# Kernel tuning notes

Hardware: AMD Instinct MI355X
Metric: run time of the kernel (lower is better)

The kernel has to match this reference:

```python
import jax, jax.numpy as jnp
import numpy as np

N, E, G = 50000, 500000, 64
DIN, ED, H1, H2, HD, OUT = 128, 32, 256, 128, 64, 8


def setup_inputs() -> dict:
    key = jax.random.key(0)
    ks = jax.random.split(key, 20)
    g = lambda i, shape: (jax.random.normal(ks[i], shape, jnp.float32) * 0.05)
    return dict(
        node_attr=jax.random.normal(ks[0], (N, DIN), jnp.float32),
        edge_attr=jax.random.normal(ks[1], (E, ED), jnp.float32),
        edge_src=jax.random.randint(ks[2], (E,), 0, N, jnp.int32),
        edge_dst=jax.random.randint(ks[3], (E,), 0, N, jnp.int32),
        batch=jnp.sort(jax.random.randint(ks[4], (N,), 0, G, jnp.int32)),
        Wl1=g(5, (DIN, H1)), bl1=jnp.zeros((H1,), jnp.float32),
        Wr1=g(6, (DIN, H1)), br1=jnp.zeros((H1,), jnp.float32),
        We1=g(7, (ED, H1)), att1=g(8, (H1,)), b1=jnp.zeros((H1,), jnp.float32),
        Wl2=g(9, (H1, H2)), bl2=jnp.zeros((H2,), jnp.float32),
        Wr2=g(10, (H1, H2)), br2=jnp.zeros((H2,), jnp.float32),
        We2=g(11, (ED, H2)), att2=g(12, (H2,)), b2=jnp.zeros((H2,), jnp.float32),
        Wd1=g(13, (H2, HD)), bd1=jnp.zeros((HD,), jnp.float32),
        bn_gamma=jnp.ones((HD,), jnp.float32), bn_beta=jnp.zeros((HD,), jnp.float32),
        bn_mean=jnp.zeros((HD,), jnp.float32), bn_var=jnp.ones((HD,), jnp.float32),
        Wd2=g(14, (HD, OUT)), bd2=jnp.zeros((OUT,), jnp.float32),
    )


def gatv2(x, src, dst, eattr, Wl, bl, Wr, br, We, att, bias, n):
    # PyG GATv2Conv, heads=1: add self-loops (fill_value='mean' for edge_attr)
    ones = jnp.ones((eattr.shape[0],), x.dtype)
    deg = jax.ops.segment_sum(ones, dst, n)
    loop_attr = jax.ops.segment_sum(eattr, dst, n) / jnp.maximum(deg, 1.0)[:, None]
    loop = jnp.arange(n, dtype=src.dtype)
    src_ = jnp.concatenate([src, loop])
    dst_ = jnp.concatenate([dst, loop])
    eattr_ = jnp.concatenate([eattr, loop_attr], axis=0)
    xl = x @ Wl + bl  # [n, C] source transform (lin_l)
    xr = x @ Wr + br  # [n, C] dest transform (lin_r)
    # edge-wise GATv2 score: a^T LeakyReLU(xl_j + xr_i + We e_ij)
    e = jax.nn.leaky_relu(xl[src_] + xr[dst_] + eattr_ @ We, 0.2) @ att  # [E+n]
    m = jax.ops.segment_max(e, dst_, n)
    w = jnp.exp(e - m[dst_])
    denom = jax.ops.segment_sum(w, dst_, n)
    alpha = w / denom[dst_]
    return jax.ops.segment_sum(alpha[:, None] * xl[src_], dst_, n) + bias


def reference(node_attr, edge_attr, edge_src, edge_dst, batch,
              Wl1, bl1, Wr1, br1, We1, att1, b1,
              Wl2, bl2, Wr2, br2, We2, att2, b2,
              Wd1, bd1, bn_gamma, bn_beta, bn_mean, bn_var, Wd2, bd2):
    x = jax.nn.relu(gatv2(node_attr, edge_src, edge_dst, edge_attr,
                          Wl1, bl1, Wr1, br1, We1, att1, b1, N))
    x = jax.nn.relu(gatv2(x, edge_src, edge_dst, edge_attr,
                          Wl2, bl2, Wr2, br2, We2, att2, b2, N))
    # global mean pool over graphs
    cnt = jax.ops.segment_sum(jnp.ones((N,), x.dtype), batch, G)
    x = jax.ops.segment_sum(x, batch, G) / jnp.maximum(cnt, 1.0)[:, None]
    x = x @ Wd1 + bd1
    # BatchNorm1d in eval mode (running stats); dropout is identity in eval
    x = (x - bn_mean) / jnp.sqrt(bn_var + 1e-5) * bn_gamma + bn_beta
    x = jax.nn.leaky_relu(x, 0.1)
    return x @ Wd2 + bd2
```

## Files before the change

### kernel.cpp

```cpp
#include <hip/hip_runtime.h>
#include <cstdint>
#include <cstddef>
#include <cmath>

constexpr int Nn = 50000;
constexpr int Ne = 500000;
constexpr int Gg = 64;
constexpr int DIN = 128, ED = 32, H1 = 256, H2 = 128, HD = 64, NOUT = 8;

typedef __attribute__((ext_vector_type(8))) short bf16x8;
typedef __attribute__((ext_vector_type(4))) float f32x4;

__device__ __forceinline__ unsigned short f2bf(float x) {
    unsigned u = __float_as_uint(x);
    u += 0x7FFFu + ((u >> 16) & 1u);
    return (unsigned short)(u >> 16);
}
__device__ __forceinline__ float bf2f(unsigned short h) {
    return __uint_as_float(((unsigned)h) << 16);
}

__global__ void count_deg_kernel(const int* __restrict__ dst, int* __restrict__ deg) {
    int e = blockIdx.x * 256 + threadIdx.x;
    if (e < Ne) atomicAdd(&deg[dst[e]], 1);
}

__global__ __launch_bounds__(1024) void scan_kernel(const int* __restrict__ deg,
                                                    int* __restrict__ row_start) {
    __shared__ int part[1024];
    int t = threadIdx.x;
    const int chunk = (Nn + 1023) / 1024;
    int lo = t * chunk;
    int hi = min(lo + chunk, Nn);
    int s = 0;
    for (int i = lo; i < hi; i++) s += deg[i];
    part[t] = s;
    __syncthreads();
    for (int off = 1; off < 1024; off <<= 1) {
        int add = (t >= off) ? part[t - off] : 0;
        __syncthreads();
        part[t] += add;
        __syncthreads();
    }
    int base = (t == 0) ? 0 : part[t - 1];
    for (int i = lo; i < hi; i++) { row_start[i] = base; base += deg[i]; }
    if (t == 0) row_start[Nn] = Ne;
}

__global__ void scatter_kernel(const int* __restrict__ dst, const int* __restrict__ row_start,
                               int* __restrict__ cursor, int* __restrict__ perm) {
    int e = blockIdx.x * 256 + threadIdx.x;
    if (e < Ne) {
        int d = dst[e];
        int p = atomicAdd(&cursor[d], 1);
        perm[row_start[d] + p] = e;
    }
}

__global__ void build_sd_kernel(const int* __restrict__ perm, const int* __restrict__ src,
                                const int* __restrict__ dst,
                                int* __restrict__ srcv, int* __restrict__ dstv) {
    int j = blockIdx.x * 256 + threadIdx.x;
    if (j < Ne) {
        int e = perm[j];
        srcv[j] = src[e];
        dstv[j] = dst[e];
    }
}

__global__ void loop_attr_kernel(const int* __restrict__ row_start, const int* __restrict__ perm,
                                 const float* __restrict__ eattr, float* __restrict__ loop_attr) {
    int tid = blockIdx.x * 256 + threadIdx.x;
    if (tid >= Nn * 8) return;
    int i = tid >> 3, q = (tid & 7) << 2;
    int r0 = row_start[i], r1 = row_start[i + 1];
    float4 s = make_float4(0.f, 0.f, 0.f, 0.f);
    for (int j = r0; j < r1; j++) {
        int e = perm[j];
        float4 v = *(const float4*)(eattr + (size_t)e * ED + q);
        s.x += v.x; s.y += v.y; s.z += v.z; s.w += v.w;
    }
    float inv = 1.0f / fmaxf((float)(r1 - r0), 1.0f);
    *(float4*)(loop_attr + (size_t)i * ED + q) =
        make_float4(s.x * inv, s.y * inv, s.z * inv, s.w * inv);
}

__global__ void cvt_split_kernel(const float* __restrict__ src,
                                 unsigned short* __restrict__ hi,
                                 unsigned short* __restrict__ lo, int n4) {
    int idx = blockIdx.x * 256 + threadIdx.x;
    if (idx >= n4) return;
    float4 v = *(const float4*)(src + (size_t)idx * 4);
    float x[4] = {v.x, v.y, v.z, v.w};
    unsigned short h[4], l[4];
#pragma unroll
    for (int c = 0; c < 4; c++) {
        h[c] = f2bf(x[c]);
        l[c] = f2bf(x[c] - bf2f(h[c]));
    }
    *(ushort4*)(hi + (size_t)idx * 4) = make_ushort4(h[0], h[1], h[2], h[3]);
    *(ushort4*)(lo + (size_t)idx * 4) = make_ushort4(l[0], l[1], l[2], l[3]);
}

__global__ void cvt_wt_kernel(const float* __restrict__ W,
                              unsigned short* __restrict__ hi,
                              unsigned short* __restrict__ lo, int K, int N) {
    int t = blockIdx.x * 256 + threadIdx.x;
    if (t >= K * N) return;
    int col = t / K, k = t % K;
    float x = W[(size_t)k * N + col];
    unsigned short h = f2bf(x);
    hi[t] = h;
    lo[t] = f2bf(x - bf2f(h));
}

template <int K, int N>
__global__ __launch_bounds__(256) void gemm_mfma_kernel(
    int M, const float* __restrict__ A,
    const unsigned short* __restrict__ wt0hi, const unsigned short* __restrict__ wt0lo,
    const float* __restrict__ bias0, float* __restrict__ C0,
    const unsigned short* __restrict__ wt1hi, const unsigned short* __restrict__ wt1lo,
    const float* __restrict__ bias1, float* __restrict__ C1) {
    const unsigned short* wthi = blockIdx.z ? wt1hi : wt0hi;
    const unsigned short* wtlo = blockIdx.z ? wt1lo : wt0lo;
    const float* bias = blockIdx.z ? bias1 : bias0;
    float* Cc = blockIdx.z ? C1 : C0;
    constexpr int KC = (K > 128) ? 128 : K;
    constexpr int P = KC + 8;
    constexpr int NT = N / 64;
    constexpr int CH = KC / 4;
    __shared__ unsigned short Ah[64 * P], Al[64 * P];
    const int tid = threadIdx.x;
    const int m0 = blockIdx.y * 64;

    const int wv = tid >> 6, lane = tid & 63;
    const int g = lane >> 4, li = lane & 15;
    const int nb = wv * (N / 4);

    f32x4 acc[4][NT];
#pragma unroll
    for (int n = 0; n < NT; n++) {
        float bc = bias[nb + n * 16 + li];
#pragma unroll
        for (int m = 0; m < 4; m++) {
            acc[m][n][0] = bc; acc[m][n][1] = bc; acc[m][n][2] = bc; acc[m][n][3] = bc;
        }
    }

    for (int kc = 0; kc < K; kc += KC) {
        for (int t = tid; t < 64 * CH; t += 256) {
            int row = t / CH, c = t % CH;
            int gr = min(m0 + row, M - 1);
            float4 v = *(const float4*)(A + (size_t)gr * K + kc + c * 4);
            unsigned short h0 = f2bf(v.x), h1 = f2bf(v.y), h2 = f2bf(v.z), h3 = f2bf(v.w);
            unsigned short l0 = f2bf(v.x - bf2f(h0)), l1 = f2bf(v.y - bf2f(h1));
            unsigned short l2 = f2bf(v.z - bf2f(h2)), l3 = f2bf(v.w - bf2f(h3));
            *(ushort4*)&Ah[row * P + c * 4] = make_ushort4(h0, h1, h2, h3);
            *(ushort4*)&Al[row * P + c * 4] = make_ushort4(l0, l1, l2, l3);
        }
        __syncthreads();

#pragma unroll
        for (int kt = 0; kt < KC / 32; kt++) {
            bf16x8 afh[4], afl[4], bfh[NT], bfl[NT];
#pragma unroll
            for (int m = 0; m < 4; m++) {
                afh[m] = *(const bf16x8*)&Ah[(m * 16 + li) * P + kt * 32 + g * 8];
                afl[m] = *(const bf16x8*)&Al[(m * 16 + li) * P + kt * 32 + g * 8];
            }
#pragma unroll
            for (int n = 0; n < NT; n++) {
                int col = nb + n * 16 + li;
                bfh[n] = *(const bf16x8*)(wthi + (size_t)col * K + kc + kt * 32 + g * 8);
                bfl[n] = *(const bf16x8*)(wtlo + (size_t)col * K + kc + kt * 32 + g * 8);
            }
#pragma unroll
            for (int m = 0; m < 4; m++)
#pragma unroll
                for (int n = 0; n < NT; n++) {
                    acc[m][n] = __builtin_amdgcn_mfma_f32_16x16x32_bf16(afh[m], bfh[n], acc[m][n], 0, 0, 0);
                    acc[m][n] = __builtin_amdgcn_mfma_f32_16x16x32_bf16(afh[m], bfl[n], acc[m][n], 0, 0, 0);
                    acc[m][n] = __builtin_amdgcn_mfma_f32_16x16x32_bf16(afl[m], bfh[n], acc[m][n], 0, 0, 0);
                }
        }
        __syncthreads();
    }

#pragma unroll
    for (int m = 0; m < 4; m++)
#pragma unroll
        for (int n = 0; n < NT; n++) {
            int col = nb + n * 16 + li;
#pragma unroll
            for (int r = 0; r < 4; r++) {
                int node = m0 + m * 16 + g * 4 + r;
                if (node < M) Cc[(size_t)node * N + col] = acc[m][n][r];
            }
        }
}

template <int C>
__global__ __launch_bounds__((C / 64) * 64) void score_mfma3_kernel(
    int count, const int* __restrict__ perm,
    const int* __restrict__ srcv, const int* __restrict__ dstv,
    const unsigned short* __restrict__ ehi, const unsigned short* __restrict__ elo,
    const float* __restrict__ xl, const float* __restrict__ xr,
    const unsigned short* __restrict__ wthi, const unsigned short* __restrict__ wtlo,
    const float* __restrict__ att, float* __restrict__ sc_out) {
    constexpr int WPB = C / 64;
    constexpr int NTHR = WPB * 64;
    __shared__ unsigned short Ah[64 * 40], Al[64 * 40];
    __shared__ float pw[WPB][64];
    const int tid = threadIdx.x;
    const int j0 = blockIdx.x * 64;

    for (int t = tid; t < 64 * 4; t += NTHR) {
        int row = t >> 2, part = t & 3;
        int j = min(j0 + row, count - 1);
        int e = perm ? perm[j] : j;
        *(uint4*)&Ah[row * 40 + part * 8] = *(const uint4*)(ehi + (size_t)e * ED + part * 8);
        *(uint4*)&Al[row * 40 + part * 8] = *(const uint4*)(elo + (size_t)e * ED + part * 8);
    }
    __syncthreads();

    const int wv = tid >> 6, lane = tid & 63;
    const int g = lane >> 4, li = lane & 15;
    const int cb = wv * 64 + g * 4;

    bf16x8 af_h[4], af_l[4];
#pragma unroll
    for (int m = 0; m < 4; m++) {
        int col = wv * 64 + m * 16 + li;
        af_h[m] = *(const bf16x8*)(wthi + (size_t)col * ED + g * 8);
        af_l[m] = *(const bf16x8*)(wtlo + (size_t)col * ED + g * 8);
    }
    float4 attv[4];
#pragma unroll
    for (int m = 0; m < 4; m++) attv[m] = *(const float4*)(att + cb + m * 16);

    int s0, d0, s1, d1, s2, d2, s3, d3;
    {
        int j;
        j = min(j0 + 0 * 16 + li, count - 1); s0 = srcv ? srcv[j] : j; d0 = dstv ? dstv[j] : j;
        j = min(j0 + 1 * 16 + li, count - 1); s1 = srcv ? srcv[j] : j; d1 = dstv ? dstv[j] : j;
        j = min(j0 + 2 * 16 + li, count - 1); s2 = srcv ? srcv[j] : j; d2 = dstv ? dstv[j] : j;
        j = min(j0 + 3 * 16 + li, count - 1); s3 = srcv ? srcv[j] : j; d3 = dstv ? dstv[j] : j;
    }

    auto pf = [&](int n, int sE, int dE, bf16x8& bh, bf16x8& bl,
                  float4 (&xlv)[4], float4 (&xrv)[4]) {
        bh = *(const bf16x8*)&Ah[(n * 16 + li) * 40 + g * 8];
        bl = *(const bf16x8*)&Al[(n * 16 + li) * 40 + g * 8];
        const float* pl = xl + (size_t)sE * C + cb;
        const float* pr = xr + (size_t)dE * C + cb;
#pragma unroll
        for (int m = 0; m < 4; m++) {
            xlv[m] = *(const float4*)(pl + m * 16);
            xrv[m] = *(const float4*)(pr + m * 16);
        }
    };
    auto comp = [&](int n, bf16x8 bh, bf16x8 bl,
                    const float4 (&xlv)[4], const float4 (&xrv)[4]) {
        f32x4 acc[4];
#pragma unroll
        for (int m = 0; m < 4; m++) {
            acc[m][0] = xlv[m].x + xrv[m].x; acc[m][1] = xlv[m].y + xrv[m].y;
            acc[m][2] = xlv[m].z + xrv[m].z; acc[m][3] = xlv[m].w + xrv[m].w;
        }
#pragma unroll
        for (int m = 0; m < 4; m++) {
            acc[m] = __builtin_amdgcn_mfma_f32_16x16x32_bf16(af_h[m], bh, acc[m], 0, 0, 0);
            acc[m] = __builtin_amdgcn_mfma_f32_16x16x32_bf16(af_h[m], bl, acc[m], 0, 0, 0);
            acc[m] = __builtin_amdgcn_mfma_f32_16x16x32_bf16(af_l[m], bh, acc[m], 0, 0, 0);
        }
        float s = 0.f;
#pragma unroll
        for (int m = 0; m < 4; m++) {
            const float av[4] = {attv[m].x, attv[m].y, attv[m].z, attv[m].w};
#pragma unroll
            for (int r = 0; r < 4; r++) {
                float z = acc[m][r];
                z = z > 0.f ? z : 0.2f * z;
                s = fmaf(z, av[r], s);
            }
        }
        s += __shfl_xor(s, 16);
        s += __shfl_xor(s, 32);
        if (lane < 16) pw[wv][n * 16 + li] = s;
    };

    bf16x8 bhA, blA, bhB, blB;
    float4 xlA[4], xrA[4], xlB[4], xrB[4];
    pf(0, s0, d0, bhA, blA, xlA, xrA);
    pf(1, s1, d1, bhB, blB, xlB, xrB);
    comp(0, bhA, blA, xlA, xrA);
    pf(2, s2, d2, bhA, blA, xlA, xrA);
    comp(1, bhB, blB, xlB, xrB);
    pf(3, s3, d3, bhB, blB, xlB, xrB);
    comp(2, bhA, blA, xlA, xrA);
    comp(3, bhB, blB, xlB, xrB);

    __syncthreads();
    if (tid < 64) {
        float s = pw[0][tid];
#pragma unroll
        for (int w = 1; w < WPB; w++) s += pw[w][tid];
        int j = j0 + tid;
        if (j < count) sc_out[j] = s;
    }
}

template <int C>
__global__ __launch_bounds__(256) void aggregate2_kernel(
    const int* __restrict__ row_start, const int* __restrict__ srcv,
    const float* __restrict__ scores, const float* __restrict__ sscore,
    const float* __restrict__ xl, const float* __restrict__ bias,
    float* __restrict__ xout) {
    constexpr int VP = C / 64;
    const int wave = threadIdx.x >> 6, lane = threadIdx.x & 63;
    const int i = blockIdx.x * 4 + wave;
    if (i >= Nn) return;
    const int r0 = row_start[i], r1 = row_start[i + 1];

    float mx = sscore[i];
    for (int j = r0 + lane; j < r1; j += 64) mx = fmaxf(mx, scores[j]);
#pragma unroll
    for (int off = 32; off >= 1; off >>= 1) mx = fmaxf(mx, __shfl_xor(mx, off));

    float l = 0.f;
    float acc[VP];
#pragma unroll
    for (int j = 0; j < VP; j++) acc[j] = 0.f;

    float wA[4], xA[4][VP];
    auto load_batch = [&](int j0, float* w, float (*x)[VP]) {
#pragma unroll
        for (int q = 0; q < 4; q++) {
            int j = min(j0 + q, r1 - 1);
            w[q] = scores[j];
            const float* p = xl + (size_t)srcv[j] * C + lane * VP;
            if constexpr (VP == 4) {
                float4 v = *(const float4*)p;
                x[q][0] = v.x; x[q][1] = v.y; x[q][2] = v.z; x[q][3] = v.w;
            } else {
                float2 v = *(const float2*)p;
                x[q][0] = v.x; x[q][1] = v.y;
            }
        }
    };
    if (r0 < r1) load_batch(r0, wA, xA);

    for (int j0 = r0; j0 < r1; j0 += 4) {
        float wB[4], xB[4][VP];
        if (j0 + 4 < r1) load_batch(j0 + 4, wB, xB);
        const int nb = min(4, r1 - j0);
        for (int q = 0; q < nb; q++) {
            float w = __expf(wA[q] - mx);
            l += w;
#pragma unroll
            for (int j = 0; j < VP; j++) acc[j] = fmaf(w, xA[q][j], acc[j]);
        }
        if (j0 + 4 < r1) {
#pragma unroll
            for (int q = 0; q < 4; q++) {
                wA[q] = wB[q];
#pragma unroll
                for (int j = 0; j < VP; j++) xA[q][j] = xB[q][j];
            }
        }
    }

    {
        float w = __expf(sscore[i] - mx);
        l += w;
        const float* p = xl + (size_t)i * C + lane * VP;
        if constexpr (VP == 4) {
            float4 v = *(const float4*)p;
            acc[0] = fmaf(w, v.x, acc[0]); acc[1] = fmaf(w, v.y, acc[1]);
            acc[2] = fmaf(w, v.z, acc[2]); acc[3] = fmaf(w, v.w, acc[3]);
        } else {
            float2 v = *(const float2*)p;
            acc[0] = fmaf(w, v.x, acc[0]); acc[1] = fmaf(w, v.y, acc[1]);
        }
    }

    float invl = 1.0f / l;
    float* xo = xout + (size_t)i * C + lane * VP;
    if constexpr (VP == 4) {
        float4 bv = *(const float4*)(bias + lane * 4);
        float4 o;
        o.x = fmaxf(fmaf(acc[0], invl, bv.x), 0.f);
        o.y = fmaxf(fmaf(acc[1], invl, bv.y), 0.f);
        o.z = fmaxf(fmaf(acc[2], invl, bv.z), 0.f);
        o.w = fmaxf(fmaf(acc[3], invl, bv.w), 0.f);
        *(float4*)xo = o;
    } else {
        float2 bv = *(const float2*)(bias + lane * 2);
        float2 o;
        o.x = fmaxf(fmaf(acc[0], invl, bv.x), 0.f);
        o.y = fmaxf(fmaf(acc[1], invl, bv.y), 0.f);
        *(float2*)xo = o;
    }
}

__global__ __launch_bounds__(128) void pool2_kernel(const float* __restrict__ x2,
                                                    const int* __restrict__ batch,
                                                    float* __restrict__ pooled,
                                                    float* __restrict__ cnt) {
    const int c = threadIdx.x;
    const int chunk = (Nn + gridDim.x - 1) / gridDim.x;
    int lo = blockIdx.x * chunk;
    int hi = min(lo + chunk, Nn);
    if (lo >= hi) return;
    int gcur = batch[lo];
    float acc = 0.f, ncnt = 0.f;
    for (int i = lo; i < hi; i++) {
        int g = batch[i];
        if (g != gcur) {
            atomicAdd(&pooled[gcur * H2 + c], acc);
            if (c == 0) atomicAdd(&cnt[gcur], ncnt);
            acc = 0.f; ncnt = 0.f; gcur = g;
        }
        acc += x2[(size_t)i * H2 + c];
        ncnt += 1.f;
    }
    atomicAdd(&pooled[gcur * H2 + c], acc);
    if (c == 0) atomicAdd(&cnt[gcur], ncnt);
}

__global__ __launch_bounds__(64) void head_kernel(
    const float* __restrict__ pooled, const float* __restrict__ cnt,
    const float* __restrict__ Wd1, const float* __restrict__ bd1,
    const float* __restrict__ gamma, const float* __restrict__ beta,
    const float* __restrict__ mean, const float* __restrict__ var,
    const float* __restrict__ Wd2, const float* __restrict__ bd2,
    float* __restrict__ out) {
    __shared__ float xm[H2];
    __shared__ float h[HD];
    int g = blockIdx.x, t = threadIdx.x;
    float c = fmaxf(cnt[g], 1.0f);
    for (int i = t; i < H2; i += 64) xm[i] = pooled[g * H2 + i] / c;
    __syncthreads();
    float a = bd1[t];
    for (int k = 0; k < H2; k++) a = fmaf(xm[k], Wd1[k * HD + t], a);
    a = (a - mean[t]) / sqrtf(var[t] + 1e-5f) * gamma[t] + beta[t];
    a = a > 0.f ? a : 0.1f * a;
    h[t] = a;
    __syncthreads();
    if (t < NOUT) {
        float o = bd2[t];
        for (int k = 0; k < HD; k++) o = fmaf(h[k], Wd2[k * NOUT + t], o);
        out[g * NOUT + t] = o;
    }
}

extern "C" void kernel_launch(void* const* d_in, const int* in_sizes, int n_in,
                              void* d_out, int out_size, void* d_ws, size_t ws_size,
                              hipStream_t stream) {
    const float* node_attr = (const float*)d_in[0];
    const float* edge_attr = (const float*)d_in[1];
    const int* edge_src = (const int*)d_in[2];
    const int* edge_dst = (const int*)d_in[3];
    const int* batch = (const int*)d_in[4];
    const float* Wl1 = (const float*)d_in[5];  const float* bl1 = (const float*)d_in[6];
    const float* Wr1 = (const float*)d_in[7];  const float* br1 = (const float*)d_in[8];
    const float* We1 = (const float*)d_in[9];  const float* att1 = (const float*)d_in[10];
    const float* b1 = (const float*)d_in[11];
    const float* Wl2 = (const float*)d_in[12]; const float* bl2 = (const float*)d_in[13];
    const float* Wr2 = (const float*)d_in[14]; const float* br2 = (const float*)d_in[15];
    const float* We2 = (const float*)d_in[16]; const float* att2 = (const float*)d_in[17];
    const float* b2 = (const float*)d_in[18];
    const float* Wd1 = (const float*)d_in[19]; const float* bd1 = (const float*)d_in[20];
    const float* bn_gamma = (const float*)d_in[21]; const float* bn_beta = (const float*)d_in[22];
    const float* bn_mean = (const float*)d_in[23];  const float* bn_var = (const float*)d_in[24];
    const float* Wd2 = (const float*)d_in[25]; const float* bd2 = (const float*)d_in[26];
    float* out = (float*)d_out;

    char* ws = (char*)d_ws;
    size_t off = 0;
    auto alloc = [&](size_t bytes) -> char* {
        char* p = ws + off;
        off = (off + bytes + 255) & ~(size_t)255;
        return p;
    };
    int* deg         = (int*)alloc((size_t)Nn * 4);
    int* row_start   = (int*)alloc((size_t)(Nn + 1) * 4);
    int* cursor      = (int*)alloc((size_t)Nn * 4);
    int* perm        = (int*)alloc((size_t)Ne * 4);
    int* srcv        = (int*)alloc((size_t)Ne * 4);
    int* dstv        = (int*)alloc((size_t)Ne * 4);
    float* loop_attr = (float*)alloc((size_t)Nn * ED * 4);
    float* scores    = (float*)alloc((size_t)Ne * 4);
    float* sscore    = (float*)alloc((size_t)Nn * 4);
    float* pooled    = (float*)alloc((size_t)Gg * H2 * 4);
    float* cnt       = (float*)alloc((size_t)Gg * 4);
    float* xlb       = (float*)alloc((size_t)Nn * H1 * 4);
    float* xrb       = (float*)alloc((size_t)Nn * H1 * 4);
    float* x1        = (float*)alloc((size_t)Nn * H1 * 4);
    unsigned short* ehi = (unsigned short*)alloc((size_t)Ne * ED * 2);
    unsigned short* elo = (unsigned short*)alloc((size_t)Ne * ED * 2);
    unsigned short* lhi = (unsigned short*)alloc((size_t)Nn * ED * 2);
    unsigned short* llo = (unsigned short*)alloc((size_t)Nn * ED * 2);
    unsigned short* w1hi = (unsigned short*)alloc((size_t)H1 * ED * 2);
    unsigned short* w1lo = (unsigned short*)alloc((size_t)H1 * ED * 2);
    unsigned short* w2hi = (unsigned short*)alloc((size_t)H2 * ED * 2);
    unsigned short* w2lo = (unsigned short*)alloc((size_t)H2 * ED * 2);
    unsigned short* wl1hi = (unsigned short*)alloc((size_t)H1 * DIN * 2);
    unsigned short* wl1lo = (unsigned short*)alloc((size_t)H1 * DIN * 2);
    unsigned short* wr1hi = (unsigned short*)alloc((size_t)H1 * DIN * 2);
    unsigned short* wr1lo = (unsigned short*)alloc((size_t)H1 * DIN * 2);
    unsigned short* wl2hi = (unsigned short*)alloc((size_t)H2 * H1 * 2);
    unsigned short* wl2lo = (unsigned short*)alloc((size_t)H2 * H1 * 2);
    unsigned short* wr2hi = (unsigned short*)alloc((size_t)H2 * H1 * 2);
    unsigned short* wr2lo = (unsigned short*)alloc((size_t)H2 * H1 * 2);

    hipMemsetAsync(deg, 0, (size_t)Nn * 4, stream);
    hipMemsetAsync(cursor, 0, (size_t)Nn * 4, stream);
    hipMemsetAsync(pooled, 0, (size_t)Gg * H2 * 4, stream);
    hipMemsetAsync(cnt, 0, (size_t)Gg * 4, stream);

    count_deg_kernel<<<(Ne + 255) / 256, 256, 0, stream>>>(edge_dst, deg);
    scan_kernel<<<1, 1024, 0, stream>>>(deg, row_start);
    scatter_kernel<<<(Ne + 255) / 256, 256, 0, stream>>>(edge_dst, row_start, cursor, perm);
    build_sd_kernel<<<(Ne + 255) / 256, 256, 0, stream>>>(perm, edge_src, edge_dst, srcv, dstv);
    loop_attr_kernel<<<(Nn * 8 + 255) / 256, 256, 0, stream>>>(row_start, perm, edge_attr, loop_attr);

    cvt_split_kernel<<<(Ne * 8 + 255) / 256, 256, 0, stream>>>(edge_attr, ehi, elo, Ne * 8);
    cvt_split_kernel<<<(Nn * 8 + 255) / 256, 256, 0, stream>>>(loop_attr, lhi, llo, Nn * 8);
    cvt_wt_kernel<<<(H1 * ED + 255) / 256, 256, 0, stream>>>(We1, w1hi, w1lo, ED, H1);
    cvt_wt_kernel<<<(H2 * ED + 255) / 256, 256, 0, stream>>>(We2, w2hi, w2lo, ED, H2);
    cvt_wt_kernel<<<(DIN * H1 + 255) / 256, 256, 0, stream>>>(Wl1, wl1hi, wl1lo, DIN, H1);
    cvt_wt_kernel<<<(DIN * H1 + 255) / 256, 256, 0, stream>>>(Wr1, wr1hi, wr1lo, DIN, H1);
    cvt_wt_kernel<<<(H1 * H2 + 255) / 256, 256, 0, stream>>>(Wl2, wl2hi, wl2lo, H1, H2);
    cvt_wt_kernel<<<(H1 * H2 + 255) / 256, 256, 0, stream>>>(Wr2, wr2hi, wr2lo, H1, H2);

    const int eb64 = (Ne + 63) / 64, nb64 = (Nn + 63) / 64;
    const int gb = (Nn + 63) / 64;

    gemm_mfma_kernel<DIN, H1><<<dim3(1, gb, 2), 256, 0, stream>>>(
        Nn, node_attr, wl1hi, wl1lo, bl1, xlb, wr1hi, wr1lo, br1, xrb);
    score_mfma3_kernel<H1><<<eb64, 256, 0, stream>>>(
        Ne, perm, srcv, dstv, ehi, elo, xlb, xrb, w1hi, w1lo, att1, scores);
    score_mfma3_kernel<H1><<<nb64, 256, 0, stream>>>(
        Nn, nullptr, nullptr, nullptr, lhi, llo, xlb, xrb, w1hi, w1lo, att1, sscore);
    aggregate2_kernel<H1><<<(Nn + 3) / 4, 256, 0, stream>>>(
        row_start, srcv, scores, sscore, xlb, b1, x1);

    gemm_mfma_kernel<H1, H2><<<dim3(1, gb, 2), 256, 0, stream>>>(
        Nn, x1, wl2hi, wl2lo, bl2, xlb, wr2hi, wr2lo, br2, xrb);
    score_mfma3_kernel<H2><<<eb64, 128, 0, stream>>>(
        Ne, perm, srcv, dstv, ehi, elo, xlb, xrb, w2hi, w2lo, att2, scores);
    score_mfma3_kernel<H2><<<nb64, 128, 0, stream>>>(
        Nn, nullptr, nullptr, nullptr, lhi, llo, xlb, xrb, w2hi, w2lo, att2, sscore);
    float* x2 = x1;
    aggregate2_kernel<H2><<<(Nn + 3) / 4, 256, 0, stream>>>(
        row_start, srcv, scores, sscore, xlb, b2, x2);

    pool2_kernel<<<256, 128, 0, stream>>>(x2, batch, pooled, cnt);
    head_kernel<<<Gg, 64, 0, stream>>>(pooled, cnt, Wd1, bd1, bn_gamma, bn_beta,
                                       bn_mean, bn_var, Wd2, bd2, out);
}
```

Measured before the change: 844.9 us.

## Fuse bf16 hi/lo split into score kernel and merge launches

Removes the separate passes that split edge and loop attributes into bf16 hi/lo arrays. The score kernel now reads fp32 attributes and does the split while staging them into shared memory. The edge and self-loop score launches are merged into one grid, and the six weight-conversion kernels become a single 2D launch. This drops the extra attribute read/write traffic and several launches. In exchange each layer's score kernel reads fp32 attributes (twice the bytes of the bf16 pair) and repeats the conversion arithmetic.

```diff
diff --git a/kernel.cpp b/kernel.cpp
--- a/kernel.cpp
+++ b/kernel.cpp
@@ -85,26 +85,22 @@
         make_float4(s.x * inv, s.y * inv, s.z * inv, s.w * inv);
 }
 
-__global__ void cvt_split_kernel(const float* __restrict__ src,
-                                 unsigned short* __restrict__ hi,
-                                 unsigned short* __restrict__ lo, int n4) {
-    int idx = blockIdx.x * 256 + threadIdx.x;
-    if (idx >= n4) return;
-    float4 v = *(const float4*)(src + (size_t)idx * 4);
-    float x[4] = {v.x, v.y, v.z, v.w};
-    unsigned short h[4], l[4];
-#pragma unroll
-    for (int c = 0; c < 4; c++) {
-        h[c] = f2bf(x[c]);
-        l[c] = f2bf(x[c] - bf2f(h[c]));
-    }
-    *(ushort4*)(hi + (size_t)idx * 4) = make_ushort4(h[0], h[1], h[2], h[3]);
-    *(ushort4*)(lo + (size_t)idx * 4) = make_ushort4(l[0], l[1], l[2], l[3]);
-}
-
-__global__ void cvt_wt_kernel(const float* __restrict__ W,
-                              unsigned short* __restrict__ hi,
-                              unsigned short* __restrict__ lo, int K, int N) {
+__global__ void cvt_wt6_kernel(
+    const float* __restrict__ We1, unsigned short* __restrict__ w1hi, unsigned short* __restrict__ w1lo,
+    const float* __restrict__ We2, unsigned short* __restrict__ w2hi, unsigned short* __restrict__ w2lo,
+    const float* __restrict__ Wl1, unsigned short* __restrict__ wl1hi, unsigned short* __restrict__ wl1lo,
+    const float* __restrict__ Wr1, unsigned short* __restrict__ wr1hi, unsigned short* __restrict__ wr1lo,
+    const float* __restrict__ Wl2, unsigned short* __restrict__ wl2hi, unsigned short* __restrict__ wl2lo,
+    const float* __restrict__ Wr2, unsigned short* __restrict__ wr2hi, unsigned short* __restrict__ wr2lo) {
+    const float* W; unsigned short *hi, *lo; int K, N;
+    switch (blockIdx.y) {
+        case 0: W = We1; hi = w1hi;  lo = w1lo;  K = ED;  N = H1; break;
+        case 1: W = We2; hi = w2hi;  lo = w2lo;  K = ED;  N = H2; break;
+        case 2: W = Wl1; hi = wl1hi; lo = wl1lo; K = DIN; N = H1; break;
+        case 3: W = Wr1; hi = wr1hi; lo = wr1lo; K = DIN; N = H1; break;
+        case 4: W = Wl2; hi = wl2hi; lo = wl2lo; K = H1;  N = H2; break;
+        default: W = Wr2; hi = wr2hi; lo = wr2lo; K = H1;  N = H2; break;
+    }
     int t = blockIdx.x * 256 + threadIdx.x;
     if (t >= K * N) return;
     int col = t / K, k = t % K;
@@ -200,26 +196,36 @@
 }
 
 template <int C>
-__global__ __launch_bounds__((C / 64) * 64) void score_mfma3_kernel(
-    int count, const int* __restrict__ perm,
+__global__ __launch_bounds__((C / 64) * 64) void score_mfma4_kernel(
+    int ecount, int eblocks, const int* __restrict__ perm,
     const int* __restrict__ srcv, const int* __restrict__ dstv,
-    const unsigned short* __restrict__ ehi, const unsigned short* __restrict__ elo,
+    const float* __restrict__ eattr, float* __restrict__ esc,
+    int ncount, const float* __restrict__ lattr, float* __restrict__ nsc,
     const float* __restrict__ xl, const float* __restrict__ xr,
     const unsigned short* __restrict__ wthi, const unsigned short* __restrict__ wtlo,
-    const float* __restrict__ att, float* __restrict__ sc_out) {
+    const float* __restrict__ att) {
     constexpr int WPB = C / 64;
     constexpr int NTHR = WPB * 64;
     __shared__ unsigned short Ah[64 * 40], Al[64 * 40];
     __shared__ float pw[WPB][64];
     const int tid = threadIdx.x;
-    const int j0 = blockIdx.x * 64;
-
-    for (int t = tid; t < 64 * 4; t += NTHR) {
-        int row = t >> 2, part = t & 3;
+    const bool selfp = (int)blockIdx.x >= eblocks;
+    const int bid = selfp ? ((int)blockIdx.x - eblocks) : (int)blockIdx.x;
+    const int count = selfp ? ncount : ecount;
+    const float* attr = selfp ? lattr : eattr;
+    float* sc_out = selfp ? nsc : esc;
+    const int j0 = bid * 64;
+
+    for (int t = tid; t < 64 * 8; t += NTHR) {
+        int row = t >> 3, c = t & 7;
         int j = min(j0 + row, count - 1);
-        int e = perm ? perm[j] : j;
-        *(uint4*)&Ah[row * 40 + part * 8] = *(const uint4*)(ehi + (size_t)e * ED + part * 8);
-        *(uint4*)&Al[row * 40 + part * 8] = *(const uint4*)(elo + (size_t)e * ED + part * 8);
+        int e = selfp ? j : perm[j];
+        float4 v = *(const float4*)(attr + (size_t)e * ED + c * 4);
+        unsigned short h0 = f2bf(v.x), h1 = f2bf(v.y), h2 = f2bf(v.z), h3 = f2bf(v.w);
+        unsigned short l0 = f2bf(v.x - bf2f(h0)), l1 = f2bf(v.y - bf2f(h1));
+        unsigned short l2 = f2bf(v.z - bf2f(h2)), l3 = f2bf(v.w - bf2f(h3));
+        *(ushort4*)&Ah[row * 40 + c * 4] = make_ushort4(h0, h1, h2, h3);
+        *(ushort4*)&Al[row * 40 + c * 4] = make_ushort4(l0, l1, l2, l3);
     }
     __syncthreads();
 
@@ -241,10 +247,14 @@
     int s0, d0, s1, d1, s2, d2, s3, d3;
     {
         int j;
-        j = min(j0 + 0 * 16 + li, count - 1); s0 = srcv ? srcv[j] : j; d0 = dstv ? dstv[j] : j;
-        j = min(j0 + 1 * 16 + li, count - 1); s1 = srcv ? srcv[j] : j; d1 = dstv ? dstv[j] : j;
-        j = min(j0 + 2 * 16 + li, count - 1); s2 = srcv ? srcv[j] : j; d2 = dstv ? dstv[j] : j;
-        j = min(j0 + 3 * 16 + li, count - 1); s3 = srcv ? srcv[j] : j; d3 = dstv ? dstv[j] : j;
+        j = min(j0 + 0 * 16 + li, count - 1);
+        s0 = selfp ? j : srcv[j]; d0 = selfp ? j : dstv[j];
+        j = min(j0 + 1 * 16 + li, count - 1);
+        s1 = selfp ? j : srcv[j]; d1 = selfp ? j : dstv[j];
+        j = min(j0 + 2 * 16 + li, count - 1);
+        s2 = selfp ? j : srcv[j]; d2 = selfp ? j : dstv[j];
+        j = min(j0 + 3 * 16 + li, count - 1);
+        s3 = selfp ? j : srcv[j]; d3 = selfp ? j : dstv[j];
     }
 
     auto pf = [&](int n, int sE, int dE, bf16x8& bh, bf16x8& bl,
@@ -497,10 +507,6 @@
     float* xlb       = (float*)alloc((size_t)Nn * H1 * 4);
     float* xrb       = (float*)alloc((size_t)Nn * H1 * 4);
     float* x1        = (float*)alloc((size_t)Nn * H1 * 4);
-    unsigned short* ehi = (unsigned short*)alloc((size_t)Ne * ED * 2);
-    unsigned short* elo = (unsigned short*)alloc((size_t)Ne * ED * 2);
-    unsigned short* lhi = (unsigned short*)alloc((size_t)Nn * ED * 2);
-    unsigned short* llo = (unsigned short*)alloc((size_t)Nn * ED * 2);
     unsigned short* w1hi = (unsigned short*)alloc((size_t)H1 * ED * 2);
     unsigned short* w1lo = (unsigned short*)alloc((size_t)H1 * ED * 2);
     unsigned short* w2hi = (unsigned short*)alloc((size_t)H2 * ED * 2);
@@ -525,33 +531,26 @@
     build_sd_kernel<<<(Ne + 255) / 256, 256, 0, stream>>>(perm, edge_src, edge_dst, srcv, dstv);
     loop_attr_kernel<<<(Nn * 8 + 255) / 256, 256, 0, stream>>>(row_start, perm, edge_attr, loop_attr);
 
-    cvt_split_kernel<<<(Ne * 8 + 255) / 256, 256, 0, stream>>>(edge_attr, ehi, elo, Ne * 8);
-    cvt_split_kernel<<<(Nn * 8 + 255) / 256, 256, 0, stream>>>(loop_attr, lhi, llo, Nn * 8);
-    cvt_wt_kernel<<<(H1 * ED + 255) / 256, 256, 0, stream>>>(We1, w1hi, w1lo, ED, H1);
-    cvt_wt_kernel<<<(H2 * ED + 255) / 256, 256, 0, stream>>>(We2, w2hi, w2lo, ED, H2);
-    cvt_wt_kernel<<<(DIN * H1 + 255) / 256, 256, 0, stream>>>(Wl1, wl1hi, wl1lo, DIN, H1);
-    cvt_wt_kernel<<<(DIN * H1 + 255) / 256, 256, 0, stream>>>(Wr1, wr1hi, wr1lo, DIN, H1);
-    cvt_wt_kernel<<<(H1 * H2 + 255) / 256, 256, 0, stream>>>(Wl2, wl2hi, wl2lo, H1, H2);
-    cvt_wt_kernel<<<(H1 * H2 + 255) / 256, 256, 0, stream>>>(Wr2, wr2hi, wr2lo, H1, H2);
+    cvt_wt6_kernel<<<dim3((DIN * H1 + 255) / 256, 6), 256, 0, stream>>>(
+        We1, w1hi, w1lo, We2, w2hi, w2lo, Wl1, wl1hi, wl1lo,
+        Wr1, wr1hi, wr1lo, Wl2, wl2hi, wl2lo, Wr2, wr2hi, wr2lo);
 
     const int eb64 = (Ne + 63) / 64, nb64 = (Nn + 63) / 64;
     const int gb = (Nn + 63) / 64;
 
     gemm_mfma_kernel<DIN, H1><<<dim3(1, gb, 2), 256, 0, stream>>>(
         Nn, node_attr, wl1hi, wl1lo, bl1, xlb, wr1hi, wr1lo, br1, xrb);
-    score_mfma3_kernel<H1><<<eb64, 256, 0, stream>>>(
-        Ne, perm, srcv, dstv, ehi, elo, xlb, xrb, w1hi, w1lo, att1, scores);
-    score_mfma3_kernel<H1><<<nb64, 256, 0, stream>>>(
-        Nn, nullptr, nullptr, nullptr, lhi, llo, xlb, xrb, w1hi, w1lo, att1, sscore);
+    score_mfma4_kernel<H1><<<eb64 + nb64, 256, 0, stream>>>(
+        Ne, eb64, perm, srcv, dstv, edge_attr, scores,
+        Nn, loop_attr, sscore, xlb, xrb, w1hi, w1lo, att1);
     aggregate2_kernel<H1><<<(Nn + 3) / 4, 256, 0, stream>>>(
         row_start, srcv, scores, sscore, xlb, b1, x1);
 
     gemm_mfma_kernel<H1, H2><<<dim3(1, gb, 2), 256, 0, stream>>>(
         Nn, x1, wl2hi, wl2lo, bl2, xlb, wr2hi, wr2lo, br2, xrb);
-    score_mfma3_kernel<H2><<<eb64, 128, 0, stream>>>(
-        Ne, perm, srcv, dstv, ehi, elo, xlb, xrb, w2hi, w2lo, att2, scores);
-    score_mfma3_kernel<H2><<<nb64, 128, 0, stream>>>(
-        Nn, nullptr, nullptr, nullptr, lhi, llo, xlb, xrb, w2hi, w2lo, att2, sscore);
+    score_mfma4_kernel<H2><<<eb64 + nb64, 128, 0, stream>>>(
+        Ne, eb64, perm, srcv, dstv, edge_attr, scores,
+        Nn, loop_attr, sscore, xlb, xrb, w2hi, w2lo, att2);
     float* x2 = x1;
     aggregate2_kernel<H2><<<(Nn + 3) / 4, 256, 0, stream>>>(
         row_start, srcv, scores, sscore, xlb, b2, x2);
```

New measurement: 782.6 us. 1.08x faster.
